# Kernel optimization log

Hardware: AMD Instinct MI355X
Metric: run time of the kernel (lower is better)

The kernel has to match this reference:

```python
import jax, jax.numpy as jnp
import numpy as np

S, E, H, V = 2048, 1024, 1024, 32000


def setup_inputs() -> dict:
    key = jax.random.key(0)
    ks = jax.random.split(key, 12)
    def n(k, shape, s=0.02):
        return jax.random.normal(k, shape, dtype=jnp.float32) * s
    return {
        "encoder_out": n(ks[0], (S, E), 1.0),
        "word_input": jax.random.randint(ks[1], (1,), 0, V),
        "last_context": n(ks[2], (1, H), 1.0),
        "h0": jnp.zeros((1, 1, H), jnp.float32),
        "c0": jnp.zeros((1, 1, H), jnp.float32),
        "emb": n(ks[3], (V, E)),
        "W_ih": n(ks[4], (4 * H, E + H)),
        "b_ih": jnp.zeros((4 * H,), jnp.float32),
        "W_hh": n(ks[5], (4 * H, H)),
        "b_hh": jnp.zeros((4 * H,), jnp.float32),
        "W_att": n(ks[6], (H, E + H)),
        "b_att": jnp.zeros((H,), jnp.float32),
        "v": jax.random.uniform(ks[7], (H,), dtype=jnp.float32) * 0.1,
        "W_ah": n(ks[8], (H, E + H)),
        "b_ah": jnp.zeros((H,), jnp.float32),
        "W_out": n(ks[9], (V, H)),
        "b_out": jnp.zeros((V,), jnp.float32),
    }


def reference(encoder_out, word_input, last_context, h0, c0, emb,
              W_ih, b_ih, W_hh, b_hh, W_att, b_att, v, W_ah, b_ah,
              W_out, b_out):
    # --- single LSTM step (torch gate order: i, f, g, o) ---
    x_emb = emb[word_input[0]]                         # [E]
    lstm_in = jnp.concatenate([last_context[0], x_emb])  # [E+H]
    gates = W_ih @ lstm_in + b_ih + W_hh @ h0[0, 0] + b_hh  # [4H]
    i, f, g, o = jnp.split(gates, 4)
    i = jax.nn.sigmoid(i); f = jax.nn.sigmoid(f)
    g = jnp.tanh(g);       o = jax.nn.sigmoid(o)
    c = f * c0[0, 0] + i * g                           # [H]
    h = o * jnp.tanh(c)                                # [H] (dropout: eval = identity)

    # --- batched additive (Bahdanau-style) attention over all S steps ---
    cat = jnp.concatenate([jnp.broadcast_to(h[None, :], (S, H)), encoder_out], axis=1)  # [S, H+E]
    scores = jnp.tanh(cat @ W_att.T + b_att) @ v       # [S]
    w = jax.nn.softmax(scores)                         # [S]
    context = w @ encoder_out                          # [E]

    # --- output projection ---
    x_t = jnp.tanh(W_ah @ jnp.concatenate([context, h]) + b_ah)  # [H]
    output = jax.nn.log_softmax(W_out @ x_t + b_out)[None, :]    # [1, V]
    return (output, (h[None, None, :], c[None, None, :]), x_t[None, :], w[None, :])
```

## Files before the change

kernel.cpp:

```cpp
#include <hip/hip_runtime.h>
#include <math.h>

typedef unsigned short u16;
typedef unsigned int u32;

typedef float  floatx4 __attribute__((ext_vector_type(4)));
typedef short  shortx8 __attribute__((ext_vector_type(8)));

#define S_LEN 2048
#define E_DIM 1024
#define H_DIM 1024
#define V_DIM 32000

#define OUT_LOG 0
#define OUT_H   32000
#define OUT_C   33024
#define OUT_XT  34048
#define OUT_W   35072

#define WS_UB     0
#define WS_SCORES 1024
#define WS_CTX    3072
#define WS_EXPSUM 4097
#define WS_ENC16  4608
#define WS_W16    (4608 + 1048576)

__device__ __forceinline__ u16 f2bf_fast(float f) {
    union { float f; u32 i; } v; v.f = f;
    return (u16)((v.i + 0x8000u) >> 16);
}
__device__ __forceinline__ float red16_sum(float x) {
    #pragma unroll
    for (int m = 1; m <= 8; m <<= 1) x += __shfl_xor(x, m, 64);
    return x;
}
__device__ __forceinline__ float wave_sum(float x) {
    #pragma unroll
    for (int m = 32; m >= 1; m >>= 1) x += __shfl_xor(x, m, 64);
    return x;
}
__device__ __forceinline__ float wave_max(float x) {
    #pragma unroll
    for (int m = 32; m >= 1; m >>= 1) x = fmaxf(x, __shfl_xor(x, m, 64));
    return x;
}
__device__ __forceinline__ float dot4(float4 a, float4 b) {
    return a.x * b.x + a.y * b.y + a.z * b.z + a.w * b.w;
}
__device__ __forceinline__ void cvt8(u16* t, float4 a, float4 b) {
    t[0] = f2bf_fast(a.x); t[1] = f2bf_fast(a.y);
    t[2] = f2bf_fast(a.z); t[3] = f2bf_fast(a.w);
    t[4] = f2bf_fast(b.x); t[5] = f2bf_fast(b.y);
    t[6] = f2bf_fast(b.z); t[7] = f2bf_fast(b.w);
}

__global__ __launch_bounds__(256) void k_lstm(
    const float* __restrict__ last_ctx, const int* __restrict__ word,
    const float* __restrict__ emb, const float* __restrict__ h0,
    const float* __restrict__ c0,
    const float* __restrict__ W_ih, const float* __restrict__ b_ih,
    const float* __restrict__ W_hh, const float* __restrict__ b_hh,
    float* __restrict__ out_h, float* __restrict__ out_c)
{
    __shared__ float gsh[4];
    int tid = threadIdx.x;
    int g = tid >> 6, l = tid & 63;
    int j = blockIdx.x;
    int row = g * H_DIM + j;
    const float* embrow = emb + (size_t)word[0] * E_DIM;
    const float* wrow = W_ih + (size_t)row * (E_DIM + H_DIM);
    const float* hrow = W_hh + (size_t)row * H_DIM;
    int c4 = l * 4;

    float s = 0.f;
    #pragma unroll
    for (int it = 0; it < 4; ++it) {
        int col = it * 256 + c4;
        s += dot4(*(const float4*)(wrow + col), *(const float4*)(last_ctx + col));
    }
    #pragma unroll
    for (int it = 0; it < 4; ++it) {
        int col = it * 256 + c4;
        s += dot4(*(const float4*)(wrow + 1024 + col), *(const float4*)(embrow + col));
    }
    #pragma unroll
    for (int it = 0; it < 4; ++it) {
        int col = it * 256 + c4;
        s += dot4(*(const float4*)(hrow + col), *(const float4*)(h0 + col));
    }
    s = wave_sum(s);
    if (l == 0) gsh[g] = s + b_ih[row] + b_hh[row];
    __syncthreads();
    if (tid == 0) {
        float gi = 1.f / (1.f + expf(-gsh[0]));
        float gf = 1.f / (1.f + expf(-gsh[1]));
        float gg = tanhf(gsh[2]);
        float go = 1.f / (1.f + expf(-gsh[3]));
        float c = gf * c0[j] + gi * gg;
        float h = go * tanhf(c);
        out_h[j] = h;
        out_c[j] = c;
    }
}

__global__ __launch_bounds__(256) void k_uproj(
    const float* __restrict__ W_att, const float* __restrict__ b_att,
    const float* __restrict__ out_h, const float* __restrict__ enc,
    float* __restrict__ wsf)
{
    int tid = threadIdx.x;
    int b = blockIdx.x;
    int gid = b * 256 + tid;
    if (gid < S_LEN) wsf[WS_SCORES + gid] = 0.f;
    else if (gid < S_LEN + E_DIM) wsf[WS_CTX + gid - S_LEN] = 0.f;
    else if (gid == S_LEN + E_DIM) wsf[WS_EXPSUM] = 0.f;

    int w = tid >> 6, l = tid & 63;
    int r = b * 4 + w;
    const float* wrow = W_att + (size_t)r * (E_DIM + H_DIM);
    int c4 = l * 4;
    float s = 0.f;
    #pragma unroll
    for (int it = 0; it < 4; ++it) {
        int col = it * 256 + c4;
        s += dot4(*(const float4*)(wrow + col), *(const float4*)(out_h + col));
    }
    s = wave_sum(s);
    if (l == 0) wsf[WS_UB + r] = s + b_att[r];

    u16* enc16 = (u16*)(wsf + WS_ENC16);
    u16* w16   = (u16*)(wsf + WS_W16);
    {
        int row = b * 8 + (tid >> 5);
        int col = (tid & 31) * 32;
        const float* src = enc + (size_t)row * E_DIM + col;
        u16 t[32];
        #pragma unroll
        for (int m = 0; m < 32; m += 8) {
            float4 x = *(const float4*)(src + m);
            float4 y = *(const float4*)(src + m + 4);
            cvt8(t + m, x, y);
        }
        uint4* dst = (uint4*)(enc16 + (size_t)row * E_DIM + col);
        #pragma unroll
        for (int m = 0; m < 4; ++m) dst[m] = *(uint4*)(t + m * 8);
    }
    {
        int row = b * 4 + (tid >> 6);
        int col = (tid & 63) * 16;
        const float* src = W_att + (size_t)row * (E_DIM + H_DIM) + H_DIM + col;
        u16 t[16];
        float4 x0 = *(const float4*)(src);
        float4 x1 = *(const float4*)(src + 4);
        float4 x2 = *(const float4*)(src + 8);
        float4 x3 = *(const float4*)(src + 12);
        cvt8(t, x0, x1); cvt8(t + 8, x2, x3);
        uint4* dst = (uint4*)(w16 + (size_t)row * E_DIM + col);
        dst[0] = *(uint4*)(t);
        dst[1] = *(uint4*)(t + 8);
    }
}

#define LDS_P 40
__global__ __launch_bounds__(256) void k_att_scores(
    const u16* __restrict__ enc16, const u16* __restrict__ w16,
    const float* __restrict__ vvec, const float* __restrict__ ws_ub,
    float* __restrict__ ws_scores)
{
    __shared__ u16 lds_a[2][128 * LDS_P];
    __shared__ u16 lds_b[2][64 * LDS_P];

    int tid = threadIdx.x;
    int w = tid >> 6, l = tid & 63;
    int b = blockIdx.x;
    int s0 = (b & 15) * 128;
    int r0 = (b >> 4) * 64;
    int lrow = l & 15, lq = l >> 4;

    int arow = tid >> 1, acol = (tid & 1) * 16;
    int brow = tid >> 2, bcol = (tid & 3) * 8;
    const u16* pa_base = enc16 + (size_t)(s0 + arow) * E_DIM + acol;
    const u16* pb_base = w16 + (size_t)(r0 + brow) * E_DIM + bcol;

    floatx4 acc[2][4];
    #pragma unroll
    for (int sf = 0; sf < 2; ++sf)
        #pragma unroll
        for (int i = 0; i < 4; ++i) acc[sf][i] = (floatx4)0.f;

    {
        uint4 a0 = *(const uint4*)(pa_base);
        uint4 a1 = *(const uint4*)(pa_base + 8);
        uint4 b0 = *(const uint4*)(pb_base);
        *(uint4*)&lds_a[0][arow * LDS_P + acol]     = a0;
        *(uint4*)&lds_a[0][arow * LDS_P + acol + 8] = a1;
        *(uint4*)&lds_b[0][brow * LDS_P + bcol]     = b0;
    }
    __syncthreads();

    int cur = 0;
    for (int kc = 0; kc < 32; ++kc) {
        uint4 nA0, nA1, nB0;
        if (kc < 31) {
            const u16* pa = pa_base + (kc + 1) * 32;
            nA0 = *(const uint4*)(pa);
            nA1 = *(const uint4*)(pa + 8);
            nB0 = *(const uint4*)(pb_base + (kc + 1) * 32);
        }

        shortx8 afrag0 = *(const shortx8*)&lds_a[cur][(w * 32 + lrow) * LDS_P + lq * 8];
        shortx8 afrag1 = *(const shortx8*)&lds_a[cur][(w * 32 + 16 + lrow) * LDS_P + lq * 8];
        #pragma unroll
        for (int rc = 0; rc < 4; ++rc) {
            shortx8 bfrag = *(const shortx8*)&lds_b[cur][(rc * 16 + lrow) * LDS_P + lq * 8];
            acc[0][rc] = __builtin_amdgcn_mfma_f32_16x16x32_bf16(afrag0, bfrag, acc[0][rc], 0, 0, 0);
            acc[1][rc] = __builtin_amdgcn_mfma_f32_16x16x32_bf16(afrag1, bfrag, acc[1][rc], 0, 0, 0);
        }

        if (kc < 31) {
            int nb = cur ^ 1;
            *(uint4*)&lds_a[nb][arow * LDS_P + acol]     = nA0;
            *(uint4*)&lds_a[nb][arow * LDS_P + acol + 8] = nA1;
            *(uint4*)&lds_b[nb][brow * LDS_P + bcol]     = nB0;
        }
        __syncthreads();
        cur ^= 1;
    }

    float part[2][4] = {{0.f,0.f,0.f,0.f},{0.f,0.f,0.f,0.f}};
    #pragma unroll
    for (int rc = 0; rc < 4; ++rc) {
        int r = r0 + rc * 16 + lrow;
        float ubr = ws_ub[r];
        float vr  = vvec[r];
        #pragma unroll
        for (int sf = 0; sf < 2; ++sf)
            #pragma unroll
            for (int reg = 0; reg < 4; ++reg)
                part[sf][reg] += tanhf(acc[sf][rc][reg] + ubr) * vr;
    }
    #pragma unroll
    for (int m = 1; m <= 8; m <<= 1)
        #pragma unroll
        for (int sf = 0; sf < 2; ++sf)
            #pragma unroll
            for (int reg = 0; reg < 4; ++reg)
                part[sf][reg] += __shfl_xor(part[sf][reg], m, 64);
    if (lrow == 0) {
        #pragma unroll
        for (int sf = 0; sf < 2; ++sf) {
            int sbase = s0 + w * 32 + sf * 16 + lq * 4;
            #pragma unroll
            for (int reg = 0; reg < 4; ++reg)
                atomicAdd(&ws_scores[sbase + reg], part[sf][reg]);
        }
    }
}

__global__ __launch_bounds__(256) void k_ctx(
    const float* __restrict__ enc, const float* __restrict__ ws_scores,
    float* __restrict__ out_w, float* __restrict__ ws_ctx)
{
    __shared__ float red[4];
    __shared__ float w_lds[16];
    __shared__ float bM, bS;
    int tid = threadIdx.x, b = blockIdx.x;

    float4 sa = *(const float4*)(ws_scores + tid * 8);
    float4 sb = *(const float4*)(ws_scores + tid * 8 + 4);
    float m = fmaxf(fmaxf(fmaxf(sa.x, sa.y), fmaxf(sa.z, sa.w)),
                    fmaxf(fmaxf(sb.x, sb.y), fmaxf(sb.z, sb.w)));
    m = wave_max(m);
    if ((tid & 63) == 0) red[tid >> 6] = m;
    __syncthreads();
    if (tid == 0) bM = fmaxf(fmaxf(red[0], red[1]), fmaxf(red[2], red[3]));
    __syncthreads();
    float M = bM;
    float e = expf(sa.x - M) + expf(sa.y - M) + expf(sa.z - M) + expf(sa.w - M)
            + expf(sb.x - M) + expf(sb.y - M) + expf(sb.z - M) + expf(sb.w - M);
    e = wave_sum(e);
    if ((tid & 63) == 0) red[tid >> 6] = e;
    __syncthreads();
    if (tid == 0) bS = red[0] + red[1] + red[2] + red[3];
    __syncthreads();
    float inv = 1.f / bS;

    int sbase = b * 16;
    if (tid < 16) {
        float wt = expf(ws_scores[sbase + tid] - M) * inv;
        w_lds[tid] = wt;
        out_w[sbase + tid] = wt;
    }
    __syncthreads();

    int e4 = tid * 4;
    float a0 = 0.f, a1 = 0.f, a2 = 0.f, a3 = 0.f;
    #pragma unroll 4
    for (int i = 0; i < 16; ++i) {
        float wt = w_lds[i];
        float4 ev = *(const float4*)(enc + (size_t)(sbase + i) * E_DIM + e4);
        a0 += wt * ev.x; a1 += wt * ev.y; a2 += wt * ev.z; a3 += wt * ev.w;
    }
    atomicAdd(&ws_ctx[e4 + 0], a0);
    atomicAdd(&ws_ctx[e4 + 1], a1);
    atomicAdd(&ws_ctx[e4 + 2], a2);
    atomicAdd(&ws_ctx[e4 + 3], a3);
}

__global__ __launch_bounds__(256) void k_xt(
    const float* __restrict__ W_ah, const float* __restrict__ b_ah,
    const float* __restrict__ ws_ctx, const float* __restrict__ out_h,
    float* __restrict__ out_xt)
{
    int tid = threadIdx.x;
    int w = tid >> 6, l = tid & 63;
    int r = blockIdx.x * 4 + w;
    const float* wrow = W_ah + (size_t)r * (E_DIM + H_DIM);
    int c4 = l * 4;
    float s = 0.f;
    #pragma unroll
    for (int it = 0; it < 4; ++it) {
        int col = it * 256 + c4;
        s += dot4(*(const float4*)(wrow + col), *(const float4*)(ws_ctx + col));
        s += dot4(*(const float4*)(wrow + 1024 + col), *(const float4*)(out_h + col));
    }
    s = wave_sum(s);
    if (l == 0) out_xt[r] = tanhf(s + b_ah[r]);
}

__global__ __launch_bounds__(256) void k_logits(
    const float* __restrict__ W_out, const float* __restrict__ b_out,
    const float* __restrict__ out_xt,
    float* __restrict__ out_log, float* __restrict__ ws_expsum)
{
    __shared__ float red[4];
    int tid = threadIdx.x;
    int w = tid >> 6, l = tid & 63;
    int sub = l >> 4, l16 = l & 15;
    int row = blockIdx.x * 16 + w * 4 + sub;
    const float* wrow = W_out + (size_t)row * H_DIM;
    int c4 = l16 * 4;
    float s = 0.f;
    #pragma unroll 4
    for (int it = 0; it < 16; ++it) {
        int col = it * 64 + c4;
        s += dot4(*(const float4*)(wrow + col), *(const float4*)(out_xt + col));
    }
    s = red16_sum(s);
    float lg = s + b_out[row];
    float e = 0.f;
    if (l16 == 0) { out_log[row] = lg; e = expf(lg); }
    e = wave_sum(e);
    if (l == 0) red[w] = e;
    __syncthreads();
    if (tid == 0)
        atomicAdd(ws_expsum, red[0] + red[1] + red[2] + red[3]);
}

__global__ __launch_bounds__(256) void k_writeout(
    const float* __restrict__ ws_expsum, float* __restrict__ out_log)
{
    int i = blockIdx.x * 256 + threadIdx.x;
    float lz = logf(ws_expsum[0]);
    out_log[i] = out_log[i] - lz;
}

extern "C" void kernel_launch(void* const* d_in, const int* in_sizes, int n_in,
                              void* d_out, int out_size, void* d_ws, size_t ws_size,
                              hipStream_t stream) {
    const float* enc      = (const float*)d_in[0];
    const int*   word     = (const int*)d_in[1];
    const float* last_ctx = (const float*)d_in[2];
    const float* h0       = (const float*)d_in[3];
    const float* c0       = (const float*)d_in[4];
    const float* emb      = (const float*)d_in[5];
    const float* W_ih     = (const float*)d_in[6];
    const float* b_ih     = (const float*)d_in[7];
    const float* W_hh     = (const float*)d_in[8];
    const float* b_hh     = (const float*)d_in[9];
    const float* W_att    = (const float*)d_in[10];
    const float* b_att    = (const float*)d_in[11];
    const float* vvec     = (const float*)d_in[12];
    const float* W_ah     = (const float*)d_in[13];
    const float* b_ah     = (const float*)d_in[14];
    const float* W_out    = (const float*)d_in[15];
    const float* b_out    = (const float*)d_in[16];

    float* wsf = (float*)d_ws;

    float* out     = (float*)d_out;
    float* out_log = out + OUT_LOG;
    float* out_h   = out + OUT_H;
    float* out_c   = out + OUT_C;
    float* out_xt  = out + OUT_XT;
    float* out_w   = out + OUT_W;

    k_lstm<<<1024, 256, 0, stream>>>(last_ctx, word, emb, h0, c0,
                                     W_ih, b_ih, W_hh, b_hh, out_h, out_c);
    k_uproj<<<256, 256, 0, stream>>>(W_att, b_att, out_h, enc, wsf);
    k_att_scores<<<256, 256, 0, stream>>>((const u16*)(wsf + WS_ENC16),
                                          (const u16*)(wsf + WS_W16),
                                          vvec, wsf + WS_UB, wsf + WS_SCORES);
    k_ctx<<<128, 256, 0, stream>>>(enc, wsf + WS_SCORES, out_w, wsf + WS_CTX);
    k_xt<<<256, 256, 0, stream>>>(W_ah, b_ah, wsf + WS_CTX, out_h, out_xt);
    k_logits<<<2000, 256, 0, stream>>>(W_out, b_out, out_xt,
                                       out_log, wsf + WS_EXPSUM);
    k_writeout<<<125, 256, 0, stream>>>(wsf + WS_EXPSUM, out_log);
}
```

Baseline: 362.7 us.

## Fuse attention-stage kernels into one persistent kernel with grid barriers

Merges the u-projection/bf16 conversion, MFMA attention-score, softmax/context and x_t kernels into one 256-block kernel, separated by software grid barriers built on an atomic counter that k_lstm resets. The context stage is re-split from 128 blocks of 16 rows to 256 blocks of 8 rows. This removes three kernel launches and their inter-kernel gaps. In exchange it relies on all 256 blocks being co-resident, which should hold on this GPU but is not guaranteed, and it adds spin-wait and fence costs at each barrier.

```diff
diff --git a/kernel.cpp b/kernel.cpp
--- a/kernel.cpp
+++ b/kernel.cpp
@@ -22,6 +22,7 @@
 #define WS_SCORES 1024
 #define WS_CTX    3072
 #define WS_EXPSUM 4097
+#define WS_BAR    4100
 #define WS_ENC16  4608
 #define WS_W16    (4608 + 1048576)
 
@@ -52,6 +53,18 @@
     t[2] = f2bf_fast(a.z); t[3] = f2bf_fast(a.w);
     t[4] = f2bf_fast(b.x); t[5] = f2bf_fast(b.y);
     t[6] = f2bf_fast(b.z); t[7] = f2bf_fast(b.w);
+}
+
+__device__ __forceinline__ void grid_bar(u32* cnt, u32 target) {
+    __threadfence();
+    __syncthreads();
+    if (threadIdx.x == 0) {
+        __hip_atomic_fetch_add(cnt, 1u, __ATOMIC_ACQ_REL, __HIP_MEMORY_SCOPE_AGENT);
+        while (__hip_atomic_load(cnt, __ATOMIC_ACQUIRE, __HIP_MEMORY_SCOPE_AGENT) < target)
+            __builtin_amdgcn_s_sleep(8);
+    }
+    __syncthreads();
+    __threadfence();
 }
 
 __global__ __launch_bounds__(256) void k_lstm(
@@ -60,10 +73,14 @@
     const float* __restrict__ c0,
     const float* __restrict__ W_ih, const float* __restrict__ b_ih,
     const float* __restrict__ W_hh, const float* __restrict__ b_hh,
-    float* __restrict__ out_h, float* __restrict__ out_c)
+    float* __restrict__ out_h, float* __restrict__ out_c,
+    float* __restrict__ wsf)
 {
     __shared__ float gsh[4];
     int tid = threadIdx.x;
+    if (blockIdx.x == 0 && tid == 0)
+        __hip_atomic_store((u32*)(wsf + WS_BAR), 0u, __ATOMIC_RELAXED,
+                           __HIP_MEMORY_SCOPE_AGENT);
     int g = tid >> 6, l = tid & 63;
     int j = blockIdx.x;
     int row = g * H_DIM + j;
@@ -103,229 +120,231 @@
     }
 }
 
-__global__ __launch_bounds__(256) void k_uproj(
+#define LDS_P 40
+__global__ __launch_bounds__(256) void k_att_fused(
     const float* __restrict__ W_att, const float* __restrict__ b_att,
     const float* __restrict__ out_h, const float* __restrict__ enc,
+    const float* __restrict__ vvec,
+    const float* __restrict__ W_ah, const float* __restrict__ b_ah,
+    float* __restrict__ out_w, float* __restrict__ out_xt,
     float* __restrict__ wsf)
-{
-    int tid = threadIdx.x;
-    int b = blockIdx.x;
-    int gid = b * 256 + tid;
-    if (gid < S_LEN) wsf[WS_SCORES + gid] = 0.f;
-    else if (gid < S_LEN + E_DIM) wsf[WS_CTX + gid - S_LEN] = 0.f;
-    else if (gid == S_LEN + E_DIM) wsf[WS_EXPSUM] = 0.f;
-
-    int w = tid >> 6, l = tid & 63;
-    int r = b * 4 + w;
-    const float* wrow = W_att + (size_t)r * (E_DIM + H_DIM);
-    int c4 = l * 4;
-    float s = 0.f;
-    #pragma unroll
-    for (int it = 0; it < 4; ++it) {
-        int col = it * 256 + c4;
-        s += dot4(*(const float4*)(wrow + col), *(const float4*)(out_h + col));
-    }
-    s = wave_sum(s);
-    if (l == 0) wsf[WS_UB + r] = s + b_att[r];
-
-    u16* enc16 = (u16*)(wsf + WS_ENC16);
-    u16* w16   = (u16*)(wsf + WS_W16);
-    {
-        int row = b * 8 + (tid >> 5);
-        int col = (tid & 31) * 32;
-        const float* src = enc + (size_t)row * E_DIM + col;
-        u16 t[32];
-        #pragma unroll
-        for (int m = 0; m < 32; m += 8) {
-            float4 x = *(const float4*)(src + m);
-            float4 y = *(const float4*)(src + m + 4);
-            cvt8(t + m, x, y);
-        }
-        uint4* dst = (uint4*)(enc16 + (size_t)row * E_DIM + col);
-        #pragma unroll
-        for (int m = 0; m < 4; ++m) dst[m] = *(uint4*)(t + m * 8);
-    }
-    {
-        int row = b * 4 + (tid >> 6);
-        int col = (tid & 63) * 16;
-        const float* src = W_att + (size_t)row * (E_DIM + H_DIM) + H_DIM + col;
-        u16 t[16];
-        float4 x0 = *(const float4*)(src);
-        float4 x1 = *(const float4*)(src + 4);
-        float4 x2 = *(const float4*)(src + 8);
-        float4 x3 = *(const float4*)(src + 12);
-        cvt8(t, x0, x1); cvt8(t + 8, x2, x3);
-        uint4* dst = (uint4*)(w16 + (size_t)row * E_DIM + col);
-        dst[0] = *(uint4*)(t);
-        dst[1] = *(uint4*)(t + 8);
-    }
-}
-
-#define LDS_P 40
-__global__ __launch_bounds__(256) void k_att_scores(
-    const u16* __restrict__ enc16, const u16* __restrict__ w16,
-    const float* __restrict__ vvec, const float* __restrict__ ws_ub,
-    float* __restrict__ ws_scores)
 {
     __shared__ u16 lds_a[2][128 * LDS_P];
     __shared__ u16 lds_b[2][64 * LDS_P];
+    __shared__ float red[4];
+    __shared__ float w_lds[8];
+    __shared__ float bM, bS;
 
     int tid = threadIdx.x;
-    int w = tid >> 6, l = tid & 63;
     int b = blockIdx.x;
-    int s0 = (b & 15) * 128;
-    int r0 = (b >> 4) * 64;
-    int lrow = l & 15, lq = l >> 4;
-
-    int arow = tid >> 1, acol = (tid & 1) * 16;
-    int brow = tid >> 2, bcol = (tid & 3) * 8;
-    const u16* pa_base = enc16 + (size_t)(s0 + arow) * E_DIM + acol;
-    const u16* pb_base = w16 + (size_t)(r0 + brow) * E_DIM + bcol;
-
-    floatx4 acc[2][4];
-    #pragma unroll
-    for (int sf = 0; sf < 2; ++sf)
-        #pragma unroll
-        for (int i = 0; i < 4; ++i) acc[sf][i] = (floatx4)0.f;
+    u32* bar = (u32*)(wsf + WS_BAR);
+    u16* enc16 = (u16*)(wsf + WS_ENC16);
+    u16* w16   = (u16*)(wsf + WS_W16);
 
     {
-        uint4 a0 = *(const uint4*)(pa_base);
-        uint4 a1 = *(const uint4*)(pa_base + 8);
-        uint4 b0 = *(const uint4*)(pb_base);
-        *(uint4*)&lds_a[0][arow * LDS_P + acol]     = a0;
-        *(uint4*)&lds_a[0][arow * LDS_P + acol + 8] = a1;
-        *(uint4*)&lds_b[0][brow * LDS_P + bcol]     = b0;
-    }
-    __syncthreads();
-
-    int cur = 0;
-    for (int kc = 0; kc < 32; ++kc) {
-        uint4 nA0, nA1, nB0;
-        if (kc < 31) {
-            const u16* pa = pa_base + (kc + 1) * 32;
-            nA0 = *(const uint4*)(pa);
-            nA1 = *(const uint4*)(pa + 8);
-            nB0 = *(const uint4*)(pb_base + (kc + 1) * 32);
-        }
-
-        shortx8 afrag0 = *(const shortx8*)&lds_a[cur][(w * 32 + lrow) * LDS_P + lq * 8];
-        shortx8 afrag1 = *(const shortx8*)&lds_a[cur][(w * 32 + 16 + lrow) * LDS_P + lq * 8];
+        int gid = b * 256 + tid;
+        if (gid < S_LEN) wsf[WS_SCORES + gid] = 0.f;
+        else if (gid < S_LEN + E_DIM) wsf[WS_CTX + gid - S_LEN] = 0.f;
+        else if (gid == S_LEN + E_DIM) wsf[WS_EXPSUM] = 0.f;
+
+        int w = tid >> 6, l = tid & 63;
+        int r = b * 4 + w;
+        const float* wrow = W_att + (size_t)r * (E_DIM + H_DIM);
+        int c4 = l * 4;
+        float s = 0.f;
+        #pragma unroll
+        for (int it = 0; it < 4; ++it) {
+            int col = it * 256 + c4;
+            s += dot4(*(const float4*)(wrow + col), *(const float4*)(out_h + col));
+        }
+        s = wave_sum(s);
+        if (l == 0) wsf[WS_UB + r] = s + b_att[r];
+
+        {
+            int row = b * 8 + (tid >> 5);
+            int col = (tid & 31) * 32;
+            const float* src = enc + (size_t)row * E_DIM + col;
+            u16 t[32];
+            #pragma unroll
+            for (int m = 0; m < 32; m += 8) {
+                float4 x = *(const float4*)(src + m);
+                float4 y = *(const float4*)(src + m + 4);
+                cvt8(t + m, x, y);
+            }
+            uint4* dst = (uint4*)(enc16 + (size_t)row * E_DIM + col);
+            #pragma unroll
+            for (int m = 0; m < 4; ++m) dst[m] = *(uint4*)(t + m * 8);
+        }
+        {
+            int row = b * 4 + (tid >> 6);
+            int col = (tid & 63) * 16;
+            const float* src = W_att + (size_t)row * (E_DIM + H_DIM) + H_DIM + col;
+            u16 t[16];
+            float4 x0 = *(const float4*)(src);
+            float4 x1 = *(const float4*)(src + 4);
+            float4 x2 = *(const float4*)(src + 8);
+            float4 x3 = *(const float4*)(src + 12);
+            cvt8(t, x0, x1); cvt8(t + 8, x2, x3);
+            uint4* dst = (uint4*)(w16 + (size_t)row * E_DIM + col);
+            dst[0] = *(uint4*)(t);
+            dst[1] = *(uint4*)(t + 8);
+        }
+    }
+
+    grid_bar(bar, 256);
+
+    {
+        const float* ws_ub = wsf + WS_UB;
+        float* ws_scores = wsf + WS_SCORES;
+        int w = tid >> 6, l = tid & 63;
+        int s0 = (b & 15) * 128;
+        int r0 = (b >> 4) * 64;
+        int lrow = l & 15, lq = l >> 4;
+
+        int arow = tid >> 1, acol = (tid & 1) * 16;
+        int brow = tid >> 2, bcol = (tid & 3) * 8;
+        const u16* pa_base = enc16 + (size_t)(s0 + arow) * E_DIM + acol;
+        const u16* pb_base = w16 + (size_t)(r0 + brow) * E_DIM + bcol;
+
+        floatx4 acc[2][4];
+        #pragma unroll
+        for (int sf = 0; sf < 2; ++sf)
+            #pragma unroll
+            for (int i = 0; i < 4; ++i) acc[sf][i] = (floatx4)0.f;
+
+        {
+            uint4 a0 = *(const uint4*)(pa_base);
+            uint4 a1 = *(const uint4*)(pa_base + 8);
+            uint4 b0 = *(const uint4*)(pb_base);
+            *(uint4*)&lds_a[0][arow * LDS_P + acol]     = a0;
+            *(uint4*)&lds_a[0][arow * LDS_P + acol + 8] = a1;
+            *(uint4*)&lds_b[0][brow * LDS_P + bcol]     = b0;
+        }
+        __syncthreads();
+
+        int cur = 0;
+        for (int kc = 0; kc < 32; ++kc) {
+            uint4 nA0, nA1, nB0;
+            if (kc < 31) {
+                const u16* pa = pa_base + (kc + 1) * 32;
+                nA0 = *(const uint4*)(pa);
+                nA1 = *(const uint4*)(pa + 8);
+                nB0 = *(const uint4*)(pb_base + (kc + 1) * 32);
+            }
+
+            shortx8 afrag0 = *(const shortx8*)&lds_a[cur][(w * 32 + lrow) * LDS_P + lq * 8];
+            shortx8 afrag1 = *(const shortx8*)&lds_a[cur][(w * 32 + 16 + lrow) * LDS_P + lq * 8];
+            #pragma unroll
+            for (int rc = 0; rc < 4; ++rc) {
+                shortx8 bfrag = *(const shortx8*)&lds_b[cur][(rc * 16 + lrow) * LDS_P + lq * 8];
+                acc[0][rc] = __builtin_amdgcn_mfma_f32_16x16x32_bf16(afrag0, bfrag, acc[0][rc], 0, 0, 0);
+                acc[1][rc] = __builtin_amdgcn_mfma_f32_16x16x32_bf16(afrag1, bfrag, acc[1][rc], 0, 0, 0);
+            }
+
+            if (kc < 31) {
+                int nb = cur ^ 1;
+                *(uint4*)&lds_a[nb][arow * LDS_P + acol]     = nA0;
+                *(uint4*)&lds_a[nb][arow * LDS_P + acol + 8] = nA1;
+                *(uint4*)&lds_b[nb][brow * LDS_P + bcol]     = nB0;
+            }
+            __syncthreads();
+            cur ^= 1;
+        }
+
+        float part[2][4] = {{0.f,0.f,0.f,0.f},{0.f,0.f,0.f,0.f}};
         #pragma unroll
         for (int rc = 0; rc < 4; ++rc) {
-            shortx8 bfrag = *(const shortx8*)&lds_b[cur][(rc * 16 + lrow) * LDS_P + lq * 8];
-            acc[0][rc] = __builtin_amdgcn_mfma_f32_16x16x32_bf16(afrag0, bfrag, acc[0][rc], 0, 0, 0);
-            acc[1][rc] = __builtin_amdgcn_mfma_f32_16x16x32_bf16(afrag1, bfrag, acc[1][rc], 0, 0, 0);
-        }
-
-        if (kc < 31) {
-            int nb = cur ^ 1;
-            *(uint4*)&lds_a[nb][arow * LDS_P + acol]     = nA0;
-            *(uint4*)&lds_a[nb][arow * LDS_P + acol + 8] = nA1;
-            *(uint4*)&lds_b[nb][brow * LDS_P + bcol]     = nB0;
-        }
-        __syncthreads();
-        cur ^= 1;
-    }
-
-    float part[2][4] = {{0.f,0.f,0.f,0.f},{0.f,0.f,0.f,0.f}};
-    #pragma unroll
-    for (int rc = 0; rc < 4; ++rc) {
-        int r = r0 + rc * 16 + lrow;
-        float ubr = ws_ub[r];
-        float vr  = vvec[r];
-        #pragma unroll
-        for (int sf = 0; sf < 2; ++sf)
-            #pragma unroll
-            for (int reg = 0; reg < 4; ++reg)
-                part[sf][reg] += tanhf(acc[sf][rc][reg] + ubr) * vr;
-    }
-    #pragma unroll
-    for (int m = 1; m <= 8; m <<= 1)
-        #pragma unroll
-        for (int sf = 0; sf < 2; ++sf)
-            #pragma unroll
-            for (int reg = 0; reg < 4; ++reg)
-                part[sf][reg] += __shfl_xor(part[sf][reg], m, 64);
-    if (lrow == 0) {
-        #pragma unroll
-        for (int sf = 0; sf < 2; ++sf) {
-            int sbase = s0 + w * 32 + sf * 16 + lq * 4;
-            #pragma unroll
-            for (int reg = 0; reg < 4; ++reg)
-                atomicAdd(&ws_scores[sbase + reg], part[sf][reg]);
-        }
-    }
-}
-
-__global__ __launch_bounds__(256) void k_ctx(
-    const float* __restrict__ enc, const float* __restrict__ ws_scores,
-    float* __restrict__ out_w, float* __restrict__ ws_ctx)
-{
-    __shared__ float red[4];
-    __shared__ float w_lds[16];
-    __shared__ float bM, bS;
-    int tid = threadIdx.x, b = blockIdx.x;
-
-    float4 sa = *(const float4*)(ws_scores + tid * 8);
-    float4 sb = *(const float4*)(ws_scores + tid * 8 + 4);
-    float m = fmaxf(fmaxf(fmaxf(sa.x, sa.y), fmaxf(sa.z, sa.w)),
-                    fmaxf(fmaxf(sb.x, sb.y), fmaxf(sb.z, sb.w)));
-    m = wave_max(m);
-    if ((tid & 63) == 0) red[tid >> 6] = m;
-    __syncthreads();
-    if (tid == 0) bM = fmaxf(fmaxf(red[0], red[1]), fmaxf(red[2], red[3]));
-    __syncthreads();
-    float M = bM;
-    float e = expf(sa.x - M) + expf(sa.y - M) + expf(sa.z - M) + expf(sa.w - M)
-            + expf(sb.x - M) + expf(sb.y - M) + expf(sb.z - M) + expf(sb.w - M);
-    e = wave_sum(e);
-    if ((tid & 63) == 0) red[tid >> 6] = e;
-    __syncthreads();
-    if (tid == 0) bS = red[0] + red[1] + red[2] + red[3];
-    __syncthreads();
-    float inv = 1.f / bS;
-
-    int sbase = b * 16;
-    if (tid < 16) {
-        float wt = expf(ws_scores[sbase + tid] - M) * inv;
-        w_lds[tid] = wt;
-        out_w[sbase + tid] = wt;
-    }
-    __syncthreads();
-
-    int e4 = tid * 4;
-    float a0 = 0.f, a1 = 0.f, a2 = 0.f, a3 = 0.f;
-    #pragma unroll 4
-    for (int i = 0; i < 16; ++i) {
-        float wt = w_lds[i];
-        float4 ev = *(const float4*)(enc + (size_t)(sbase + i) * E_DIM + e4);
-        a0 += wt * ev.x; a1 += wt * ev.y; a2 += wt * ev.z; a3 += wt * ev.w;
-    }
-    atomicAdd(&ws_ctx[e4 + 0], a0);
-    atomicAdd(&ws_ctx[e4 + 1], a1);
-    atomicAdd(&ws_ctx[e4 + 2], a2);
-    atomicAdd(&ws_ctx[e4 + 3], a3);
-}
-
-__global__ __launch_bounds__(256) void k_xt(
-    const float* __restrict__ W_ah, const float* __restrict__ b_ah,
-    const float* __restrict__ ws_ctx, const float* __restrict__ out_h,
-    float* __restrict__ out_xt)
-{
-    int tid = threadIdx.x;
-    int w = tid >> 6, l = tid & 63;
-    int r = blockIdx.x * 4 + w;
-    const float* wrow = W_ah + (size_t)r * (E_DIM + H_DIM);
-    int c4 = l * 4;
-    float s = 0.f;
-    #pragma unroll
-    for (int it = 0; it < 4; ++it) {
-        int col = it * 256 + c4;
-        s += dot4(*(const float4*)(wrow + col), *(const float4*)(ws_ctx + col));
-        s += dot4(*(const float4*)(wrow + 1024 + col), *(const float4*)(out_h + col));
-    }
-    s = wave_sum(s);
-    if (l == 0) out_xt[r] = tanhf(s + b_ah[r]);
+            int r = r0 + rc * 16 + lrow;
+            float ubr = ws_ub[r];
+            float vr  = vvec[r];
+            #pragma unroll
+            for (int sf = 0; sf < 2; ++sf)
+                #pragma unroll
+                for (int reg = 0; reg < 4; ++reg)
+                    part[sf][reg] += tanhf(acc[sf][rc][reg] + ubr) * vr;
+        }
+        #pragma unroll
+        for (int m = 1; m <= 8; m <<= 1)
+            #pragma unroll
+            for (int sf = 0; sf < 2; ++sf)
+                #pragma unroll
+                for (int reg = 0; reg < 4; ++reg)
+                    part[sf][reg] += __shfl_xor(part[sf][reg], m, 64);
+        if (lrow == 0) {
+            #pragma unroll
+            for (int sf = 0; sf < 2; ++sf) {
+                int sbase = s0 + w * 32 + sf * 16 + lq * 4;
+                #pragma unroll
+                for (int reg = 0; reg < 4; ++reg)
+                    atomicAdd(&ws_scores[sbase + reg], part[sf][reg]);
+            }
+        }
+    }
+
+    grid_bar(bar, 512);
+
+    {
+        const float* ws_scores = wsf + WS_SCORES;
+        float* ws_ctx = wsf + WS_CTX;
+        float4 sa = *(const float4*)(ws_scores + tid * 8);
+        float4 sb = *(const float4*)(ws_scores + tid * 8 + 4);
+        float m = fmaxf(fmaxf(fmaxf(sa.x, sa.y), fmaxf(sa.z, sa.w)),
+                        fmaxf(fmaxf(sb.x, sb.y), fmaxf(sb.z, sb.w)));
+        m = wave_max(m);
+        if ((tid & 63) == 0) red[tid >> 6] = m;
+        __syncthreads();
+        if (tid == 0) bM = fmaxf(fmaxf(red[0], red[1]), fmaxf(red[2], red[3]));
+        __syncthreads();
+        float M = bM;
+        float e = expf(sa.x - M) + expf(sa.y - M) + expf(sa.z - M) + expf(sa.w - M)
+                + expf(sb.x - M) + expf(sb.y - M) + expf(sb.z - M) + expf(sb.w - M);
+        e = wave_sum(e);
+        if ((tid & 63) == 0) red[tid >> 6] = e;
+        __syncthreads();
+        if (tid == 0) bS = red[0] + red[1] + red[2] + red[3];
+        __syncthreads();
+        float inv = 1.f / bS;
+
+        int sbase = b * 8;
+        if (tid < 8) {
+            float wt = expf(ws_scores[sbase + tid] - M) * inv;
+            w_lds[tid] = wt;
+            out_w[sbase + tid] = wt;
+        }
+        __syncthreads();
+
+        int e4 = tid * 4;
+        float a0 = 0.f, a1 = 0.f, a2 = 0.f, a3 = 0.f;
+        #pragma unroll
+        for (int i = 0; i < 8; ++i) {
+            float wt = w_lds[i];
+            float4 ev = *(const float4*)(enc + (size_t)(sbase + i) * E_DIM + e4);
+            a0 += wt * ev.x; a1 += wt * ev.y; a2 += wt * ev.z; a3 += wt * ev.w;
+        }
+        atomicAdd(&ws_ctx[e4 + 0], a0);
+        atomicAdd(&ws_ctx[e4 + 1], a1);
+        atomicAdd(&ws_ctx[e4 + 2], a2);
+        atomicAdd(&ws_ctx[e4 + 3], a3);
+    }
+
+    grid_bar(bar, 768);
+
+    {
+        const float* ws_ctx = wsf + WS_CTX;
+        int w = tid >> 6, l = tid & 63;
+        int r = b * 4 + w;
+        const float* wrow = W_ah + (size_t)r * (E_DIM + H_DIM);
+        int c4 = l * 4;
+        float s = 0.f;
+        #pragma unroll
+        for (int it = 0; it < 4; ++it) {
+            int col = it * 256 + c4;
+            s += dot4(*(const float4*)(wrow + col), *(const float4*)(ws_ctx + col));
+            s += dot4(*(const float4*)(wrow + 1024 + col), *(const float4*)(out_h + col));
+        }
+        s = wave_sum(s);
+        if (l == 0) out_xt[r] = tanhf(s + b_ah[r]);
+    }
 }
 
 __global__ __launch_bounds__(256) void k_logits(
@@ -396,13 +415,9 @@
     float* out_w   = out + OUT_W;
 
     k_lstm<<<1024, 256, 0, stream>>>(last_ctx, word, emb, h0, c0,
-                                     W_ih, b_ih, W_hh, b_hh, out_h, out_c);
-    k_uproj<<<256, 256, 0, stream>>>(W_att, b_att, out_h, enc, wsf);
-    k_att_scores<<<256, 256, 0, stream>>>((const u16*)(wsf + WS_ENC16),
-                                          (const u16*)(wsf + WS_W16),
-                                          vvec, wsf + WS_UB, wsf + WS_SCORES);
-    k_ctx<<<128, 256, 0, stream>>>(enc, wsf + WS_SCORES, out_w, wsf + WS_CTX);
-    k_xt<<<256, 256, 0, stream>>>(W_ah, b_ah, wsf + WS_CTX, out_h, out_xt);
+                                     W_ih, b_ih, W_hh, b_hh, out_h, out_c, wsf);
+    k_att_fused<<<256, 256, 0, stream>>>(W_att, b_att, out_h, enc, vvec,
+                                         W_ah, b_ah, out_w, out_xt, wsf);
     k_logits<<<2000, 256, 0, stream>>>(W_out, b_out, out_xt,
                                        out_log, wsf + WS_EXPSUM);
     k_writeout<<<125, 256, 0, stream>>>(wsf + WS_EXPSUM, out_log);
```

Result: slower. 536.5 us (+47.9%).
